# Performance work log

Measured on AMD Instinct MI355X. Metric: run time of the kernel, lower is better.

## Reference

```python
import jax, jax.numpy as jnp
import numpy as np

B, T, I, H = 64, 2048, 256, 256


def setup_inputs() -> dict:
    key = jax.random.key(0)
    ks = jax.random.split(key, 9)
    s = 1.0 / np.sqrt(H).astype(np.float32)  # torch nn.RNN init: U(-1/sqrt(H), 1/sqrt(H))
    u = lambda k, shape: jax.random.uniform(k, shape, jnp.float32, -s, s)
    return {
        "input_feature": jax.random.normal(ks[0], (B, T, I), jnp.float32),
        "W_ih0": u(ks[1], (H, I)),
        "W_hh0": u(ks[2], (H, H)),
        "b_ih0": u(ks[3], (H,)),
        "b_hh0": u(ks[4], (H,)),
        "W_ih1": u(ks[5], (H, H)),
        "W_hh1": u(ks[6], (H, H)),
        "b_ih1": u(ks[7], (H,)),
        "b_hh1": u(ks[8], (H,)),
    }


def _rnn_layer(x, W_ih, W_hh, b_ih, b_hh):
    # x: [B, T, F]. Precompute the input projection for all timesteps at once,
    # then scan the recurrence: h_t = tanh(x_t W_ih^T + b_ih + h_{t-1} W_hh^T + b_hh)
    pre = jnp.einsum("btf,hf->bth", x, W_ih) + b_ih + b_hh  # [B, T, H]
    h0 = jnp.zeros((x.shape[0], W_hh.shape[0]), x.dtype)

    def step(h, p):
        h_new = jnp.tanh(p + h @ W_hh.T)
        return h_new, h_new

    _, ys = jax.lax.scan(step, h0, jnp.swapaxes(pre, 0, 1))  # [T, B, H]
    return jnp.swapaxes(ys, 0, 1)  # [B, T, H]


def reference(input_feature, W_ih0, W_hh0, b_ih0, b_hh0, W_ih1, W_hh1, b_ih1, b_hh1):
    # hidden_0 = zeros, batch_first=True, tanh nonlinearity (torch.nn.RNN default)
    h = _rnn_layer(input_feature, W_ih0, W_hh0, b_ih0, b_hh0)
    h = _rnn_layer(h, W_ih1, W_hh1, b_ih1, b_hh1)
    return h  # output: [B, T, H] (module returns only `output`)
```

## Files before the change

kernel.cpp:

```cpp
#include <hip/hip_runtime.h>
#include <stdint.h>

#define B_ 64
#define T_ 2048
#define H_ 256
#define S_ 64
#define C_ (T_ / S_)

typedef unsigned int u32;
typedef unsigned short u16;
typedef __attribute__((ext_vector_type(8))) short short8;
typedef __attribute__((ext_vector_type(4))) float f32x4;

#define SWZ(row, byte) (((row) * 512) + ((byte) ^ (((row) & 7) << 4)))

static __device__ __forceinline__ u32 cvtpk(float a, float b) {
  u32 d;
  asm("v_cvt_pk_bf16_f32 %0, %1, %2" : "=v"(d) : "v"(a), "v"(b));
  return d;
}
static __device__ __forceinline__ uint4 pack8(float4 a, float4 b) {
  uint4 r;
  r.x = cvtpk(a.x, a.y); r.y = cvtpk(a.z, a.w);
  r.z = cvtpk(b.x, b.y); r.w = cvtpk(b.z, b.w);
  return r;
}
static __device__ __forceinline__ short8 as8(uint4 v) {
  return __builtin_bit_cast(short8, v);
}
static __device__ __forceinline__ f32x4 mfma4(uint4 a, uint4 b, f32x4 c) {
  return __builtin_amdgcn_mfma_f32_16x16x32_bf16(as8(a), as8(b), c, 0, 0, 0);
}
static __device__ __forceinline__ float fast_tanh(float x) {
  float e = __expf(2.0f * x);
  float r = __builtin_amdgcn_rcpf(e + 1.0f);
  return fmaf(-2.0f, r, 1.0f);
}

template <int NQ>
static __device__ __forceinline__ void load_wfrag(const float* W, int qbase, int bl,
                                                  int g, uint4 wf[NQ][8]) {
#pragma unroll
  for (int q = 0; q < NQ; ++q) {
    const float* wr = W + (size_t)((qbase + q) * 16 + bl) * H_ + g * 8;
#pragma unroll
    for (int kc = 0; kc < 8; ++kc) {
      float4 a = *(const float4*)(wr + kc * 32);
      float4 b = *(const float4*)(wr + kc * 32 + 4);
      wf[q][kc] = pack8(a, b);
    }
  }
}

__global__ __launch_bounds__(256, 2) void pre_mfma(const float* X, const float* W,
                                                   const float* bi, const float* bh,
                                                   float* P, int tpw) {
  __shared__ char sb_[2][8192];
  const int tid = threadIdx.x;
  const int lane = tid & 63, wv = tid >> 6;
  const int bl = lane & 15, g = lane >> 4;

  uint4 wf[4][8];
  load_wfrag<4>(W, wv * 4, bl, g, wf);
  float4 bias[4];
#pragma unroll
  for (int q = 0; q < 4; ++q) {
    const int j0 = (wv * 4 + q) * 16 + g * 4;
    float4 a = *(const float4*)(bi + j0);
    float4 c = *(const float4*)(bh + j0);
    bias[q].x = a.x + c.x; bias[q].y = a.y + c.y;
    bias[q].z = a.z + c.z; bias[q].w = a.w + c.w;
  }

  const size_t row0 = (size_t)blockIdx.x * tpw * 16;
  const int sr = tid >> 4, sc = (tid & 15) * 16;
  float4 s0, s1, s2, s3;
  {
    const float4* xs = (const float4*)(X + (row0 + sr) * H_ + sc);
    s0 = xs[0]; s1 = xs[1]; s2 = xs[2]; s3 = xs[3];
  }

  for (int i = 0; i < tpw; ++i) {
    char* sb = sb_[i & 1];
    *(uint4*)(sb + SWZ(sr, sc * 2)) = pack8(s0, s1);
    *(uint4*)(sb + SWZ(sr, sc * 2 + 16)) = pack8(s2, s3);
    __syncthreads();
    if (i + 1 < tpw) {
      const float4* xn = (const float4*)(X + (row0 + (i + 1) * 16 + sr) * H_ + sc);
      s0 = xn[0]; s1 = xn[1]; s2 = xn[2]; s3 = xn[3];
    }
    uint4 hf[8];
#pragma unroll
    for (int kc = 0; kc < 8; ++kc)
      hf[kc] = *(const uint4*)(sb + SWZ(bl, kc * 64 + g * 16));
    f32x4 acc[4];
#pragma unroll
    for (int q = 0; q < 4; ++q) {
      acc[q] = (f32x4){0.f, 0.f, 0.f, 0.f};
#pragma unroll
      for (int kc = 0; kc < 8; ++kc)
        acc[q] = mfma4(wf[q][kc], hf[kc], acc[q]);
    }
#pragma unroll
    for (int q = 0; q < 4; ++q) {
      const int j0 = (wv * 4 + q) * 16 + g * 4;
      float4 o;
      o.x = acc[q][0] + bias[q].x; o.y = acc[q][1] + bias[q].y;
      o.z = acc[q][2] + bias[q].z; o.w = acc[q][3] + bias[q].w;
      *(float4*)(P + (row0 + i * 16 + bl) * H_ + j0) = o;
    }
    __syncthreads();
  }
}

__global__ __launch_bounds__(512, 1) void rec_mfma(const float* pre, const float* W,
                                                   float* out) {
  __shared__ char hb_[2][8192];
  const int tid = threadIdx.x;
  const int lane = tid & 63, wv = tid >> 6;
  const int bl = lane & 15, g = lane >> 4;
  const int b0 = blockIdx.x * 16;

  uint4 wf[2][8];
  load_wfrag<2>(W, wv * 2, bl, g, wf);
  {
    uint4 z = make_uint4(0, 0, 0, 0);
    ((uint4*)hb_[0])[tid] = z;
    ((uint4*)hb_[1])[tid] = z;
  }
  const float* prow = pre + (size_t)(b0 + bl) * T_ * H_;
  float* orow = out + (size_t)(b0 + bl) * T_ * H_;
  float4 pr0[2], pr1[2];
#pragma unroll
  for (int q = 0; q < 2; ++q) {
    const int j0 = (wv * 2 + q) * 16 + g * 4;
    pr0[q] = *(const float4*)(prow + 0 * H_ + j0);
    pr1[q] = *(const float4*)(prow + 1 * H_ + j0);
  }
  __syncthreads();

  auto step = [&](int t, float4 (&pr)[2], char* rbuf, char* wbuf) {
    uint4 hf[8];
#pragma unroll
    for (int kc = 0; kc < 8; ++kc)
      hf[kc] = *(const uint4*)(rbuf + SWZ(bl, kc * 64 + g * 16));
    f32x4 accA[2], accB[2];
#pragma unroll
    for (int q = 0; q < 2; ++q) {
      accA[q] = (f32x4){0.f, 0.f, 0.f, 0.f};
      accB[q] = (f32x4){0.f, 0.f, 0.f, 0.f};
#pragma unroll
      for (int kc = 0; kc < 4; ++kc) {
        accA[q] = mfma4(wf[q][kc], hf[kc], accA[q]);
        accB[q] = mfma4(wf[q][kc + 4], hf[kc + 4], accB[q]);
      }
    }
#pragma unroll
    for (int q = 0; q < 2; ++q) {
      const int j0 = (wv * 2 + q) * 16 + g * 4;
      const float* pq = (const float*)&pr[q];
      float v0 = fast_tanh(accA[q][0] + accB[q][0] + pq[0]);
      float v1 = fast_tanh(accA[q][1] + accB[q][1] + pq[1]);
      float v2 = fast_tanh(accA[q][2] + accB[q][2] + pq[2]);
      float v3 = fast_tanh(accA[q][3] + accB[q][3] + pq[3]);
      uint2 hw; hw.x = cvtpk(v0, v1); hw.y = cvtpk(v2, v3);
      *(uint2*)(wbuf + SWZ(bl, j0 * 2)) = hw;
      float4 o; o.x = v0; o.y = v1; o.z = v2; o.w = v3;
      *(float4*)(orow + (size_t)t * H_ + j0) = o;
      if (t + 2 < T_)
        pr[q] = *(const float4*)(prow + (size_t)(t + 2) * H_ + j0);
    }
    asm volatile("s_waitcnt lgkmcnt(0)" ::: "memory");
    __builtin_amdgcn_s_barrier();
    __builtin_amdgcn_sched_barrier(0);
  };

  for (int t = 0; t < T_; t += 2) {
    step(t, pr0, hb_[0], hb_[1]);
    step(t + 1, pr1, hb_[1], hb_[0]);
  }
}

__global__ __launch_bounds__(512, 1) void chunk2_k(
    float* dout, const float* Whh0, const float* Wih1, const float* Whh1,
    const float* bih1, const float* bhh1,
    u16* ring, u16* carry0, u16* carry1, int c) {
  __shared__ __align__(16) char smem[2 * 8192];
  const int tid = threadIdx.x;
  const int lane = tid & 63, wv = tid >> 6;
  const int bl = lane & 15, g = lane >> 4;
  const int bid = blockIdx.x;
  char* sb0 = smem;
  char* sb1 = smem + 8192;

  if (bid < 4) {
    if (c >= C_) return;
    const int pair = bid;
    uint4 wf[2][8];
    load_wfrag<2>(Whh0, wv * 2, bl, g, wf);
    if (c == 0) {
      uint4 z = make_uint4(0, 0, 0, 0);
      ((uint4*)sb0)[tid] = z;
    } else {
      const u16* cr = carry0 + pair * 16 * H_ + bl * H_;
#pragma unroll
      for (int q = 0; q < 2; ++q) {
        const int j0 = (wv * 2 + q) * 16 + g * 4;
        uint2 hw = *(const uint2*)(cr + j0);
        *(uint2*)(sb0 + SWZ(bl, j0 * 2)) = hw;
      }
    }
    const float* prow = dout + (size_t)(pair * 16 + bl) * T_ * H_ + (size_t)c * S_ * H_;
    u16* rch = ring + ((size_t)(c & 1) * S_) * (B_ * H_) + (size_t)(pair * 16 + bl) * H_;
    float4 pr0[2], pr1[2];
#pragma unroll
    for (int q = 0; q < 2; ++q) {
      const int j0 = (wv * 2 + q) * 16 + g * 4;
      pr0[q] = *(const float4*)(prow + 0 * H_ + j0);
      pr1[q] = *(const float4*)(prow + 1 * H_ + j0);
    }
    __syncthreads();

    auto step = [&](int s, float4 (&pr)[2], char* rbuf, char* wbuf) {
      uint4 hf[8];
#pragma unroll
      for (int kc = 0; kc < 8; ++kc)
        hf[kc] = *(const uint4*)(rbuf + SWZ(bl, kc * 64 + g * 16));
      f32x4 accA[2], accB[2];
#pragma unroll
      for (int q = 0; q < 2; ++q) {
        accA[q] = (f32x4){0.f, 0.f, 0.f, 0.f};
        accB[q] = (f32x4){0.f, 0.f, 0.f, 0.f};
#pragma unroll
        for (int kc = 0; kc < 4; ++kc) {
          accA[q] = mfma4(wf[q][kc], hf[kc], accA[q]);
          accB[q] = mfma4(wf[q][kc + 4], hf[kc + 4], accB[q]);
        }
      }
#pragma unroll
      for (int q = 0; q < 2; ++q) {
        const int j0 = (wv * 2 + q) * 16 + g * 4;
        const float* pq = (const float*)&pr[q];
        float v0 = fast_tanh(accA[q][0] + accB[q][0] + pq[0]);
        float v1 = fast_tanh(accA[q][1] + accB[q][1] + pq[1]);
        float v2 = fast_tanh(accA[q][2] + accB[q][2] + pq[2]);
        float v3 = fast_tanh(accA[q][3] + accB[q][3] + pq[3]);
        uint2 hw; hw.x = cvtpk(v0, v1); hw.y = cvtpk(v2, v3);
        *(uint2*)(wbuf + SWZ(bl, j0 * 2)) = hw;
        *(uint2*)(rch + (size_t)s * (B_ * H_) + j0) = hw;
        if (s + 2 < S_)
          pr[q] = *(const float4*)(prow + (size_t)(s + 2) * H_ + j0);
      }
      asm volatile("s_waitcnt lgkmcnt(0)" ::: "memory");
      __builtin_amdgcn_s_barrier();
      __builtin_amdgcn_sched_barrier(0);
    };
    for (int s = 0; s < S_; s += 2) {
      step(s, pr0, sb0, sb1);
      step(s + 1, pr1, sb1, sb0);
    }
    {
      u16* cw = carry0 + pair * 16 * H_ + bl * H_;
#pragma unroll
      for (int q = 0; q < 2; ++q) {
        const int j0 = (wv * 2 + q) * 16 + g * 4;
        uint2 hw = *(const uint2*)(sb0 + SWZ(bl, j0 * 2));
        *(uint2*)(cw + j0) = hw;
      }
    }
  } else if (bid < 8) {
    if (c < 1 || c > C_) return;
    const int pair = bid - 4;
    const int ch = c - 1;
    uint4 wf[2][8];
    load_wfrag<2>(Wih1, wv * 2, bl, g, wf);
    float4 cb[2];
#pragma unroll
    for (int q = 0; q < 2; ++q) {
      const int j0 = (wv * 2 + q) * 16 + g * 4;
      float4 a = *(const float4*)(bih1 + j0);
      float4 b = *(const float4*)(bhh1 + j0);
      cb[q].x = a.x + b.x; cb[q].y = a.y + b.y;
      cb[q].z = a.z + b.z; cb[q].w = a.w + b.w;
    }
    const u16* rbase2 = ring + ((size_t)(ch & 1) * S_) * (B_ * H_) + (size_t)pair * 16 * H_;
    const int sr = tid >> 5, scb = (tid & 31) * 16;
    uint4 v = *(const uint4*)(rbase2 + 0 * (B_ * H_) + (size_t)sr * H_ + (tid & 31) * 8);

    for (int s = 0; s < S_; ++s) {
      char* sb = (s & 1) ? sb1 : sb0;
      *(uint4*)(sb + SWZ(sr, scb)) = v;
      __syncthreads();
      if (s + 1 < S_)
        v = *(const uint4*)(rbase2 + (size_t)(s + 1) * (B_ * H_) + (size_t)sr * H_ + (tid & 31) * 8);
      uint4 hf[8];
#pragma unroll
      for (int kc = 0; kc < 8; ++kc)
        hf[kc] = *(const uint4*)(sb + SWZ(bl, kc * 64 + g * 16));
      f32x4 acc[2];
#pragma unroll
      for (int q = 0; q < 2; ++q) {
        acc[q] = (f32x4){0.f, 0.f, 0.f, 0.f};
#pragma unroll
        for (int kc = 0; kc < 8; ++kc)
          acc[q] = mfma4(wf[q][kc], hf[kc], acc[q]);
      }
      float* od = dout + (size_t)(pair * 16 + bl) * T_ * H_ + (size_t)(ch * S_ + s) * H_;
#pragma unroll
      for (int q = 0; q < 2; ++q) {
        const int j0 = (wv * 2 + q) * 16 + g * 4;
        float4 o;
        o.x = acc[q][0] + cb[q].x; o.y = acc[q][1] + cb[q].y;
        o.z = acc[q][2] + cb[q].z; o.w = acc[q][3] + cb[q].w;
        *(float4*)(od + j0) = o;
      }
      __syncthreads();
    }
  } else {
    if (c < 2) return;
    const int pair = bid - 8;
    const int ch = c - 2;
    uint4 wf[2][8];
    load_wfrag<2>(Whh1, wv * 2, bl, g, wf);
    if (ch == 0) {
      uint4 z = make_uint4(0, 0, 0, 0);
      ((uint4*)sb0)[tid] = z;
    } else {
      const u16* cr = carry1 + pair * 16 * H_ + bl * H_;
#pragma unroll
      for (int q = 0; q < 2; ++q) {
        const int j0 = (wv * 2 + q) * 16 + g * 4;
        uint2 hw = *(const uint2*)(cr + j0);
        *(uint2*)(sb0 + SWZ(bl, j0 * 2)) = hw;
      }
    }
    float* prow = dout + (size_t)(pair * 16 + bl) * T_ * H_ + (size_t)ch * S_ * H_;
    float4 pr0[2], pr1[2];
#pragma unroll
    for (int q = 0; q < 2; ++q) {
      const int j0 = (wv * 2 + q) * 16 + g * 4;
      pr0[q] = *(const float4*)(prow + 0 * H_ + j0);
      pr1[q] = *(const float4*)(prow + 1 * H_ + j0);
    }
    __syncthreads();

    auto step = [&](int s, float4 (&pr)[2], char* rbuf, char* wbuf) {
      uint4 hf[8];
#pragma unroll
      for (int kc = 0; kc < 8; ++kc)
        hf[kc] = *(const uint4*)(rbuf + SWZ(bl, kc * 64 + g * 16));
      f32x4 accA[2], accB[2];
#pragma unroll
      for (int q = 0; q < 2; ++q) {
        accA[q] = (f32x4){0.f, 0.f, 0.f, 0.f};
        accB[q] = (f32x4){0.f, 0.f, 0.f, 0.f};
#pragma unroll
        for (int kc = 0; kc < 4; ++kc) {
          accA[q] = mfma4(wf[q][kc], hf[kc], accA[q]);
          accB[q] = mfma4(wf[q][kc + 4], hf[kc + 4], accB[q]);
        }
      }
#pragma unroll
      for (int q = 0; q < 2; ++q) {
        const int j0 = (wv * 2 + q) * 16 + g * 4;
        const float* pq = (const float*)&pr[q];
        float v0 = fast_tanh(accA[q][0] + accB[q][0] + pq[0]);
        float v1 = fast_tanh(accA[q][1] + accB[q][1] + pq[1]);
        float v2 = fast_tanh(accA[q][2] + accB[q][2] + pq[2]);
        float v3 = fast_tanh(accA[q][3] + accB[q][3] + pq[3]);
        uint2 hw; hw.x = cvtpk(v0, v1); hw.y = cvtpk(v2, v3);
        *(uint2*)(wbuf + SWZ(bl, j0 * 2)) = hw;
        float4 o; o.x = v0; o.y = v1; o.z = v2; o.w = v3;
        *(float4*)(prow + (size_t)s * H_ + j0) = o;
        if (s + 2 < S_)
          pr[q] = *(const float4*)(prow + (size_t)(s + 2) * H_ + j0);
      }
      asm volatile("s_waitcnt lgkmcnt(0)" ::: "memory");
      __builtin_amdgcn_s_barrier();
      __builtin_amdgcn_sched_barrier(0);
    };
    for (int s = 0; s < S_; s += 2) {
      step(s, pr0, sb0, sb1);
      step(s + 1, pr1, sb1, sb0);
    }
    {
      u16* cw = carry1 + pair * 16 * H_ + bl * H_;
#pragma unroll
      for (int q = 0; q < 2; ++q) {
        const int j0 = (wv * 2 + q) * 16 + g * 4;
        uint2 hw = *(const uint2*)(sb0 + SWZ(bl, j0 * 2));
        *(uint2*)(cw + j0) = hw;
      }
    }
  }
}

extern "C" void kernel_launch(void* const* d_in, const int* in_sizes, int n_in,
                              void* d_out, int out_size, void* d_ws, size_t ws_size,
                              hipStream_t stream) {
  (void)in_sizes; (void)n_in; (void)out_size;
  const float* x    = (const float*)d_in[0];
  const float* Wih0 = (const float*)d_in[1];
  const float* Whh0 = (const float*)d_in[2];
  const float* bih0 = (const float*)d_in[3];
  const float* bhh0 = (const float*)d_in[4];
  const float* Wih1 = (const float*)d_in[5];
  const float* Whh1 = (const float*)d_in[6];
  const float* bih1 = (const float*)d_in[7];
  const float* bhh1 = (const float*)d_in[8];
  float* out = (float*)d_out;

  const int TPW = 8;
  const int NWG = (B_ * T_) / (TPW * 16);
  const size_t ring_elems = (size_t)2 * S_ * B_ * H_;
  const size_t carry_elems = (size_t)4 * 16 * H_;
  const size_t need = (ring_elems + 2 * carry_elems) * sizeof(u16);

  pre_mfma<<<dim3(NWG), dim3(256), 0, stream>>>(x, Wih0, bih0, bhh0, out, TPW);
  if (ws_size >= need) {
    u16* ring = (u16*)d_ws;
    u16* carry0 = ring + ring_elems;
    u16* carry1 = carry0 + carry_elems;
    for (int c = 0; c <= C_ + 1; ++c)
      chunk2_k<<<dim3(12), dim3(512), 0, stream>>>(
          out, Whh0, Wih1, Whh1, bih1, bhh1, ring, carry0, carry1, c);
  } else {
    rec_mfma<<<dim3(B_ / 16), dim3(512), 0, stream>>>(out, Whh0, out);
    pre_mfma<<<dim3(NWG), dim3(256), 0, stream>>>(out, Wih1, bih1, bhh1, out, TPW);
    rec_mfma<<<dim3(B_ / 16), dim3(512), 0, stream>>>(out, Whh1, out);
  }
}
```

Measured before the change: 2.430 ms.

## Pack two batch groups per recurrent block and unify layer recurrences

Recurrent blocks now process two 16-row batch groups each, with four waves per group and each wave computing four output column tiles instead of two. Layer-0 and layer-1 recurrence share one code path and the launch uses 8 blocks instead of 12, with the carry buffer sized for the full batch. The aim is fewer blocks and fewer waves per group exchanging state. The cost is a longer per-wave MFMA chain per timestep, more weight registers, and a block-wide barrier that couples the two groups.

```diff
diff --git a/kernel.cpp b/kernel.cpp
--- a/kernel.cpp
+++ b/kernel.cpp
@@ -181,54 +181,64 @@
   }
 }
 
-__global__ __launch_bounds__(512, 1) void chunk2_k(
+__global__ __launch_bounds__(512, 1) void chunk3_k(
     float* dout, const float* Whh0, const float* Wih1, const float* Whh1,
     const float* bih1, const float* bhh1,
     u16* ring, u16* carry0, u16* carry1, int c) {
-  __shared__ __align__(16) char smem[2 * 8192];
+  __shared__ __align__(16) char smem[4 * 8192];
   const int tid = threadIdx.x;
   const int lane = tid & 63, wv = tid >> 6;
   const int bl = lane & 15, g = lane >> 4;
   const int bid = blockIdx.x;
-  char* sb0 = smem;
-  char* sb1 = smem + 8192;
-
-  if (bid < 4) {
-    if (c >= C_) return;
-    const int pair = bid;
-    uint4 wf[2][8];
-    load_wfrag<2>(Whh0, wv * 2, bl, g, wf);
-    if (c == 0) {
+
+  if (bid < 2 || bid >= 6) {
+    const bool is0 = (bid < 2);
+    if (is0) { if (c >= C_) return; }
+    else     { if (c < 2) return; }
+    const int ch = is0 ? c : (c - 2);
+    const int grp = wv >> 2;
+    const int qb = (wv & 3) * 4;
+    const int bbase = (is0 ? bid : bid - 6) * 32 + grp * 16;
+    char* h0 = smem + grp * 16384;
+    char* h1 = h0 + 8192;
+
+    uint4 wf[4][8];
+    load_wfrag<4>(is0 ? Whh0 : Whh1, qb, bl, g, wf);
+    u16* carry = (is0 ? carry0 : carry1) + (size_t)(bbase + bl) * H_;
+
+    if (ch == 0) {
       uint4 z = make_uint4(0, 0, 0, 0);
-      ((uint4*)sb0)[tid] = z;
+      const int lt = (wv & 3) * 64 + lane;
+      ((uint4*)h0)[lt] = z;
+      ((uint4*)h0)[lt + 256] = z;
     } else {
-      const u16* cr = carry0 + pair * 16 * H_ + bl * H_;
-#pragma unroll
-      for (int q = 0; q < 2; ++q) {
-        const int j0 = (wv * 2 + q) * 16 + g * 4;
-        uint2 hw = *(const uint2*)(cr + j0);
-        *(uint2*)(sb0 + SWZ(bl, j0 * 2)) = hw;
-      }
-    }
-    const float* prow = dout + (size_t)(pair * 16 + bl) * T_ * H_ + (size_t)c * S_ * H_;
-    u16* rch = ring + ((size_t)(c & 1) * S_) * (B_ * H_) + (size_t)(pair * 16 + bl) * H_;
-    float4 pr0[2], pr1[2];
-#pragma unroll
-    for (int q = 0; q < 2; ++q) {
-      const int j0 = (wv * 2 + q) * 16 + g * 4;
+#pragma unroll
+      for (int q = 0; q < 4; ++q) {
+        const int j0 = (qb + q) * 16 + g * 4;
+        uint2 hw = *(const uint2*)(carry + j0);
+        *(uint2*)(h0 + SWZ(bl, j0 * 2)) = hw;
+      }
+    }
+
+    float* prow = dout + (size_t)(bbase + bl) * T_ * H_ + (size_t)ch * S_ * H_;
+    u16* rch = ring + ((size_t)(ch & 1) * S_) * (B_ * H_) + (size_t)(bbase + bl) * H_;
+    float4 pr0[4], pr1[4];
+#pragma unroll
+    for (int q = 0; q < 4; ++q) {
+      const int j0 = (qb + q) * 16 + g * 4;
       pr0[q] = *(const float4*)(prow + 0 * H_ + j0);
       pr1[q] = *(const float4*)(prow + 1 * H_ + j0);
     }
     __syncthreads();
 
-    auto step = [&](int s, float4 (&pr)[2], char* rbuf, char* wbuf) {
+    auto step = [&](int s, float4 (&pr)[4], char* rbuf, char* wbuf) {
       uint4 hf[8];
 #pragma unroll
       for (int kc = 0; kc < 8; ++kc)
         hf[kc] = *(const uint4*)(rbuf + SWZ(bl, kc * 64 + g * 16));
-      f32x4 accA[2], accB[2];
-#pragma unroll
-      for (int q = 0; q < 2; ++q) {
+      f32x4 accA[4], accB[4];
+#pragma unroll
+      for (int q = 0; q < 4; ++q) {
         accA[q] = (f32x4){0.f, 0.f, 0.f, 0.f};
         accB[q] = (f32x4){0.f, 0.f, 0.f, 0.f};
 #pragma unroll
@@ -238,8 +248,8 @@
         }
       }
 #pragma unroll
-      for (int q = 0; q < 2; ++q) {
-        const int j0 = (wv * 2 + q) * 16 + g * 4;
+      for (int q = 0; q < 4; ++q) {
+        const int j0 = (qb + q) * 16 + g * 4;
         const float* pq = (const float*)&pr[q];
         float v0 = fast_tanh(accA[q][0] + accB[q][0] + pq[0]);
         float v1 = fast_tanh(accA[q][1] + accB[q][1] + pq[1]);
@@ -247,7 +257,12 @@
         float v3 = fast_tanh(accA[q][3] + accB[q][3] + pq[3]);
         uint2 hw; hw.x = cvtpk(v0, v1); hw.y = cvtpk(v2, v3);
         *(uint2*)(wbuf + SWZ(bl, j0 * 2)) = hw;
-        *(uint2*)(rch + (size_t)s * (B_ * H_) + j0) = hw;
+        if (is0) {
+          *(uint2*)(rch + (size_t)s * (B_ * H_) + j0) = hw;
+        } else {
+          float4 o; o.x = v0; o.y = v1; o.z = v2; o.w = v3;
+          *(float4*)(prow + (size_t)s * H_ + j0) = o;
+        }
         if (s + 2 < S_)
           pr[q] = *(const float4*)(prow + (size_t)(s + 2) * H_ + j0);
       }
@@ -256,22 +271,23 @@
       __builtin_amdgcn_sched_barrier(0);
     };
     for (int s = 0; s < S_; s += 2) {
-      step(s, pr0, sb0, sb1);
-      step(s + 1, pr1, sb1, sb0);
+      step(s, pr0, h0, h1);
+      step(s + 1, pr1, h1, h0);
     }
     {
-      u16* cw = carry0 + pair * 16 * H_ + bl * H_;
-#pragma unroll
-      for (int q = 0; q < 2; ++q) {
-        const int j0 = (wv * 2 + q) * 16 + g * 4;
-        uint2 hw = *(const uint2*)(sb0 + SWZ(bl, j0 * 2));
-        *(uint2*)(cw + j0) = hw;
-      }
-    }
-  } else if (bid < 8) {
+#pragma unroll
+      for (int q = 0; q < 4; ++q) {
+        const int j0 = (qb + q) * 16 + g * 4;
+        uint2 hw = *(const uint2*)(h0 + SWZ(bl, j0 * 2));
+        *(uint2*)(carry + j0) = hw;
+      }
+    }
+  } else {
     if (c < 1 || c > C_) return;
-    const int pair = bid - 4;
+    const int pair = bid - 2;
     const int ch = c - 1;
+    char* sb0 = smem;
+    char* sb1 = smem + 8192;
     uint4 wf[2][8];
     load_wfrag<2>(Wih1, wv * 2, bl, g, wf);
     float4 cb[2];
@@ -315,82 +331,6 @@
         *(float4*)(od + j0) = o;
       }
       __syncthreads();
-    }
-  } else {
-    if (c < 2) return;
-    const int pair = bid - 8;
-    const int ch = c - 2;
-    uint4 wf[2][8];
-    load_wfrag<2>(Whh1, wv * 2, bl, g, wf);
-    if (ch == 0) {
-      uint4 z = make_uint4(0, 0, 0, 0);
-      ((uint4*)sb0)[tid] = z;
-    } else {
-      const u16* cr = carry1 + pair * 16 * H_ + bl * H_;
-#pragma unroll
-      for (int q = 0; q < 2; ++q) {
-        const int j0 = (wv * 2 + q) * 16 + g * 4;
-        uint2 hw = *(const uint2*)(cr + j0);
-        *(uint2*)(sb0 + SWZ(bl, j0 * 2)) = hw;
-      }
-    }
-    float* prow = dout + (size_t)(pair * 16 + bl) * T_ * H_ + (size_t)ch * S_ * H_;
-    float4 pr0[2], pr1[2];
-#pragma unroll
-    for (int q = 0; q < 2; ++q) {
-      const int j0 = (wv * 2 + q) * 16 + g * 4;
-      pr0[q] = *(const float4*)(prow + 0 * H_ + j0);
-      pr1[q] = *(const float4*)(prow + 1 * H_ + j0);
-    }
-    __syncthreads();
-
-    auto step = [&](int s, float4 (&pr)[2], char* rbuf, char* wbuf) {
-      uint4 hf[8];
-#pragma unroll
-      for (int kc = 0; kc < 8; ++kc)
-        hf[kc] = *(const uint4*)(rbuf + SWZ(bl, kc * 64 + g * 16));
-      f32x4 accA[2], accB[2];
-#pragma unroll
-      for (int q = 0; q < 2; ++q) {
-        accA[q] = (f32x4){0.f, 0.f, 0.f, 0.f};
-        accB[q] = (f32x4){0.f, 0.f, 0.f, 0.f};
-#pragma unroll
-        for (int kc = 0; kc < 4; ++kc) {
-          accA[q] = mfma4(wf[q][kc], hf[kc], accA[q]);
-          accB[q] = mfma4(wf[q][kc + 4], hf[kc + 4], accB[q]);
-        }
-      }
-#pragma unroll
-      for (int q = 0; q < 2; ++q) {
-        const int j0 = (wv * 2 + q) * 16 + g * 4;
-        const float* pq = (const float*)&pr[q];
-        float v0 = fast_tanh(accA[q][0] + accB[q][0] + pq[0]);
-        float v1 = fast_tanh(accA[q][1] + accB[q][1] + pq[1]);
-        float v2 = fast_tanh(accA[q][2] + accB[q][2] + pq[2]);
-        float v3 = fast_tanh(accA[q][3] + accB[q][3] + pq[3]);
-        uint2 hw; hw.x = cvtpk(v0, v1); hw.y = cvtpk(v2, v3);
-        *(uint2*)(wbuf + SWZ(bl, j0 * 2)) = hw;
-        float4 o; o.x = v0; o.y = v1; o.z = v2; o.w = v3;
-        *(float4*)(prow + (size_t)s * H_ + j0) = o;
-        if (s + 2 < S_)
-          pr[q] = *(const float4*)(prow + (size_t)(s + 2) * H_ + j0);
-      }
-      asm volatile("s_waitcnt lgkmcnt(0)" ::: "memory");
-      __builtin_amdgcn_s_barrier();
-      __builtin_amdgcn_sched_barrier(0);
-    };
-    for (int s = 0; s < S_; s += 2) {
-      step(s, pr0, sb0, sb1);
-      step(s + 1, pr1, sb1, sb0);
-    }
-    {
-      u16* cw = carry1 + pair * 16 * H_ + bl * H_;
-#pragma unroll
-      for (int q = 0; q < 2; ++q) {
-        const int j0 = (wv * 2 + q) * 16 + g * 4;
-        uint2 hw = *(const uint2*)(sb0 + SWZ(bl, j0 * 2));
-        *(uint2*)(cw + j0) = hw;
-      }
     }
   }
 }
@@ -413,7 +353,7 @@
   const int TPW = 8;
   const int NWG = (B_ * T_) / (TPW * 16);
   const size_t ring_elems = (size_t)2 * S_ * B_ * H_;
-  const size_t carry_elems = (size_t)4 * 16 * H_;
+  const size_t carry_elems = (size_t)B_ * H_;
   const size_t need = (ring_elems + 2 * carry_elems) * sizeof(u16);
 
   pre_mfma<<<dim3(NWG), dim3(256), 0, stream>>>(x, Wih0, bih0, bhh0, out, TPW);
@@ -422,7 +362,7 @@
     u16* carry0 = ring + ring_elems;
     u16* carry1 = carry0 + carry_elems;
     for (int c = 0; c <= C_ + 1; ++c)
-      chunk2_k<<<dim3(12), dim3(512), 0, stream>>>(
+      chunk3_k<<<dim3(8), dim3(512), 0, stream>>>(
           out, Whh0, Wih1, Whh1, bih1, bhh1, ring, carry0, carry1, c);
   } else {
     rec_mfma<<<dim3(B_ / 16), dim3(512), 0, stream>>>(out, Whh0, out);
```

New measurement: 5.545 ms. +128.2%, slower.

## Fuse layer-0 input projection into chunked pipeline, computing next chunk alongside recurrence

Applied to the files above, without the earlier changes.

Removes the standalone full-sequence layer-0 input projection kernel. A small pre-kernel now projects only chunk 0, and 32 extra workgroups in each chunk launch project chunk c+1 while the recurrence blocks process chunk c. The aim is to hide the projection's global traffic and compute behind the latency-bound recurrence, which uses only a few workgroups. The risk is that the extra workgroups compete for memory bandwidth with the serial recurrence blocks. The carry buffer sizing is also changed.

```diff
diff --git a/kernel.cpp b/kernel.cpp
--- a/kernel.cpp
+++ b/kernel.cpp
@@ -50,6 +50,78 @@
       wf[q][kc] = pack8(a, b);
     }
   }
+}
+
+static __device__ void proj0_body(char* smem, const float* X, const float* Wih0,
+                                  const float* bih0, const float* bhh0,
+                                  float* dout, int ch, int bid2) {
+  const int tid = threadIdx.x;
+  const int lane = tid & 63, wv = tid >> 6;
+  const int bl = lane & 15, g = lane >> 4;
+  char* sb0 = smem;
+  char* sb1 = smem + 8192;
+
+  uint4 wf[2][8];
+  load_wfrag<2>(Wih0, wv * 2, bl, g, wf);
+  float4 cb[2];
+#pragma unroll
+  for (int q = 0; q < 2; ++q) {
+    const int j0 = (wv * 2 + q) * 16 + g * 4;
+    float4 a = *(const float4*)(bih0 + j0);
+    float4 b = *(const float4*)(bhh0 + j0);
+    cb[q].x = a.x + b.x; cb[q].y = a.y + b.y;
+    cb[q].z = a.z + b.z; cb[q].w = a.w + b.w;
+  }
+
+  const int sr = tid >> 5, sc8 = (tid & 31) * 8;
+  auto rowbase = [&](int it) -> size_t {
+    const int b = bid2 * 2 + (it >> 2), i = it & 3;
+    return (size_t)(b * T_ + ch * S_ + i * 16);
+  };
+  float4 s0, s1;
+  {
+    const float4* xs = (const float4*)(X + (rowbase(0) + sr) * H_ + sc8);
+    s0 = xs[0]; s1 = xs[1];
+  }
+
+  for (int it = 0; it < 8; ++it) {
+    char* sb = (it & 1) ? sb1 : sb0;
+    *(uint4*)(sb + SWZ(sr, sc8 * 2)) = pack8(s0, s1);
+    __syncthreads();
+    if (it + 1 < 8) {
+      const float4* xn = (const float4*)(X + (rowbase(it + 1) + sr) * H_ + sc8);
+      s0 = xn[0]; s1 = xn[1];
+    }
+    uint4 hf[8];
+#pragma unroll
+    for (int kc = 0; kc < 8; ++kc)
+      hf[kc] = *(const uint4*)(sb + SWZ(bl, kc * 64 + g * 16));
+    f32x4 acc[2];
+#pragma unroll
+    for (int q = 0; q < 2; ++q) {
+      acc[q] = (f32x4){0.f, 0.f, 0.f, 0.f};
+#pragma unroll
+      for (int kc = 0; kc < 8; ++kc)
+        acc[q] = mfma4(wf[q][kc], hf[kc], acc[q]);
+    }
+    float* od = dout + (rowbase(it) + bl) * H_;
+#pragma unroll
+    for (int q = 0; q < 2; ++q) {
+      const int j0 = (wv * 2 + q) * 16 + g * 4;
+      float4 o;
+      o.x = acc[q][0] + cb[q].x; o.y = acc[q][1] + cb[q].y;
+      o.z = acc[q][2] + cb[q].z; o.w = acc[q][3] + cb[q].w;
+      *(float4*)(od + j0) = o;
+    }
+    __syncthreads();
+  }
+}
+
+__global__ __launch_bounds__(512, 1) void pre_chunk0(const float* X, const float* Wih0,
+                                                     const float* bih0, const float* bhh0,
+                                                     float* dout) {
+  __shared__ __align__(16) char smem[2 * 8192];
+  proj0_body(smem, X, Wih0, bih0, bhh0, dout, 0, blockIdx.x);
 }
 
 __global__ __launch_bounds__(256, 2) void pre_mfma(const float* X, const float* W,
@@ -181,8 +253,9 @@
   }
 }
 
-__global__ __launch_bounds__(512, 1) void chunk2_k(
-    float* dout, const float* Whh0, const float* Wih1, const float* Whh1,
+__global__ __launch_bounds__(512, 1) void chunk4_k(
+    const float* X, float* dout, const float* Wih0, const float* bih0,
+    const float* bhh0, const float* Whh0, const float* Wih1, const float* Whh1,
     const float* bih1, const float* bhh1,
     u16* ring, u16* carry0, u16* carry1, int c) {
   __shared__ __align__(16) char smem[2 * 8192];
@@ -316,7 +389,7 @@
       }
       __syncthreads();
     }
-  } else {
+  } else if (bid < 12) {
     if (c < 2) return;
     const int pair = bid - 8;
     const int ch = c - 2;
@@ -392,6 +465,9 @@
         *(uint2*)(cw + j0) = hw;
       }
     }
+  } else {
+    if (c + 1 > C_ - 1) return;
+    proj0_body(smem, X, Wih0, bih0, bhh0, dout, c + 1, bid - 12);
   }
 }
 
@@ -410,21 +486,23 @@
   const float* bhh1 = (const float*)d_in[8];
   float* out = (float*)d_out;
 
-  const int TPW = 8;
-  const int NWG = (B_ * T_) / (TPW * 16);
   const size_t ring_elems = (size_t)2 * S_ * B_ * H_;
-  const size_t carry_elems = (size_t)4 * 16 * H_;
+  const size_t carry_elems = (size_t)B_ * H_;
   const size_t need = (ring_elems + 2 * carry_elems) * sizeof(u16);
 
-  pre_mfma<<<dim3(NWG), dim3(256), 0, stream>>>(x, Wih0, bih0, bhh0, out, TPW);
   if (ws_size >= need) {
     u16* ring = (u16*)d_ws;
     u16* carry0 = ring + ring_elems;
     u16* carry1 = carry0 + carry_elems;
+    pre_chunk0<<<dim3(32), dim3(512), 0, stream>>>(x, Wih0, bih0, bhh0, out);
     for (int c = 0; c <= C_ + 1; ++c)
-      chunk2_k<<<dim3(12), dim3(512), 0, stream>>>(
-          out, Whh0, Wih1, Whh1, bih1, bhh1, ring, carry0, carry1, c);
+      chunk4_k<<<dim3(44), dim3(512), 0, stream>>>(
+          x, out, Wih0, bih0, bhh0, Whh0, Wih1, Whh1, bih1, bhh1,
+          ring, carry0, carry1, c);
   } else {
+    const int TPW = 8;
+    const int NWG = (B_ * T_) / (TPW * 16);
+    pre_mfma<<<dim3(NWG), dim3(256), 0, stream>>>(x, Wih0, bih0, bhh0, out, TPW);
     rec_mfma<<<dim3(B_ / 16), dim3(512), 0, stream>>>(out, Whh0, out);
     pre_mfma<<<dim3(NWG), dim3(256), 0, stream>>>(out, Wih1, bih1, bhh1, out, TPW);
     rec_mfma<<<dim3(B_ / 16), dim3(512), 0, stream>>>(out, Whh1, out);
```

After: 2.431 ms. No clear change (+0.0%).
